# Performance work log

Measured on AMD Instinct MI355X. Metric: run time of the kernel, lower is better.

## Reference

```python
import jax, jax.numpy as jnp
import numpy as np
import math

B, L, D, P = 2, 2048, 256, 32
PI = math.pi


def _layernorm(x, g, b, eps=1e-5):
    m = x.mean(-1, keepdims=True)
    v = x.var(-1, keepdims=True)
    return (x - m) / jnp.sqrt(v + eps) * g + b


def setup_inputs() -> dict:
    key = jax.random.key(0)
    ks = jax.random.split(key, 16)
    sd = 1.0 / math.sqrt(D)
    f32 = jnp.float32
    inp = {
        "x": jax.random.normal(ks[0], (B, L, D), f32),
        # key_encoder: Linear(D, P)
        "key_W": jax.random.normal(ks[1], (D, P), f32) * sd,
        "key_b": jnp.zeros((P,), f32),
        # value_encoder: Linear(D, D)
        "val_W": jax.random.normal(ks[2], (D, D), f32) * sd,
        "val_b": jnp.zeros((D,), f32),
        # refiner: LayerNorm(D), Linear(D, 2D), GELU, Linear(2D, D)
        "ln1_g": jnp.ones((D,), f32),
        "ln1_b": jnp.zeros((D,), f32),
        "W1": jax.random.normal(ks[3], (D, 2 * D), f32) * sd,
        "b1": jnp.zeros((2 * D,), f32),
        "W2": jax.random.normal(ks[4], (2 * D, D), f32) * (1.0 / math.sqrt(2 * D)),
        "b2": jnp.zeros((D,), f32),
        # to_out: LayerNorm(D), Linear(D, D)
        "ln2_g": jnp.ones((D,), f32),
        "ln2_b": jnp.zeros((D,), f32),
        "Wo": jax.random.normal(ks[5], (D, D), f32) * sd,
        "bo": jnp.zeros((D,), f32),
    }
    return inp


def reference(x, key_W, key_b, val_W, val_b, ln1_g, ln1_b, W1, b1, W2, b2,
              ln2_g, ln2_b, Wo, bo):
    # key phases in (-pi, pi); phasor exp(i*theta) handled as (cos, sin)
    phases = jnp.tanh(x @ key_W + key_b) * PI          # (B, L, P)
    values = x @ val_W + val_b                          # (B, L, D)

    cos_p = jnp.cos(phases)
    sin_p = jnp.sin(phases)
    # torch.roll(shifts=1, dims=1) then zero the first position -> shift right, row 0 = 0
    zrow = jnp.zeros_like(cos_p[:, :1])
    cos_s = jnp.concatenate([zrow, cos_p[:, :-1]], axis=1)
    sin_s = jnp.concatenate([zrow, sin_p[:, :-1]], axis=1)

    # odd positions hold values
    vmask = (jnp.arange(L) % 2 == 1).astype(x.dtype)    # (L,)
    mv = values * vmask[None, :, None]                  # (B, L, D)

    # bind: outer product phasor (P) x value (D); real/imag parts
    bound_re = cos_s[..., None] * mv[:, :, None, :]     # (B, L, P, D)
    bound_im = sin_s[..., None] * mv[:, :, None, :]
    mem_re = jnp.cumsum(bound_re, axis=1)
    mem_im = jnp.cumsum(bound_im, axis=1)

    # retrieve: Re[ memory * exp(-i*theta) ] summed over phases
    retrieved = (jnp.einsum('blpd,blp->bld', mem_re, cos_p)
                 + jnp.einsum('blpd,blp->bld', mem_im, sin_p))

    valid = jnp.maximum(jnp.cumsum(vmask), 1.0)         # (L,)
    retrieved = retrieved / (jnp.sqrt(valid)[None, :, None] * math.sqrt(P))

    h = _layernorm(retrieved, ln1_g, ln1_b)
    h = jax.nn.gelu(h @ W1 + b1, approximate=False)
    refined = h @ W2 + b2
    out = x + (_layernorm(refined, ln2_g, ln2_b) @ Wo + bo)
    return out
```

## Files before the change

kernel.cpp:

```cpp
#include <hip/hip_runtime.h>
#include <math.h>

#define BB 2
#define LL 2048
#define DD 256
#define PP 32
#define NC 64
#define PI_F 3.14159265358979323846f

typedef __attribute__((ext_vector_type(8))) short bf16x8;
typedef __attribute__((ext_vector_type(4))) float f32x4;
typedef unsigned short ushort_t;
typedef unsigned int uint_t;

__device__ inline ushort_t f2bf(float x) {
    uint_t u = __float_as_uint(x);
    uint_t r = (u + 0x7fffu + ((u >> 16) & 1u)) >> 16;
    return (ushort_t)r;
}

__global__ __launch_bounds__(256) void prep_key_kernel(
    const float* __restrict__ W1, const float* __restrict__ W2,
    const float* __restrict__ Wo, const float* __restrict__ valW,
    const float* __restrict__ x, const float* __restrict__ key_W,
    const float* __restrict__ key_b,
    ushort_t* __restrict__ W1t, ushort_t* __restrict__ W2t,
    ushort_t* __restrict__ Wot, ushort_t* __restrict__ valWt,
    float2* __restrict__ ph)
{
    const int bid = blockIdx.x;
    const int t = threadIdx.x;
    if (bid < 96) {
        __shared__ float T[64][65];
        const float* W; ushort_t* Wt; int K, N, tile;
        if (bid < 32)      { W = W1;   Wt = W1t;   K = 256; N = 512; tile = bid; }
        else if (bid < 64) { W = W2;   Wt = W2t;   K = 512; N = 256; tile = bid - 32; }
        else if (bid < 80) { W = Wo;   Wt = Wot;   K = 256; N = 256; tile = bid - 64; }
        else               { W = valW; Wt = valWt; K = 256; N = 256; tile = bid - 80; }
        const int ntiles = N / 64;
        const int k0 = (tile / ntiles) * 64, n0 = (tile % ntiles) * 64;
        {
            const int rr = t >> 2, cb = (t & 3) * 16;
            #pragma unroll
            for (int i = 0; i < 16; i += 4) {
                const float4 v = *(const float4*)&W[(k0 + rr) * N + n0 + cb + i];
                T[rr][cb + i + 0] = v.x; T[rr][cb + i + 1] = v.y;
                T[rr][cb + i + 2] = v.z; T[rr][cb + i + 3] = v.w;
            }
        }
        __syncthreads();
        {
            const int n = t >> 2, kb = (t & 3) * 16;
            #pragma unroll
            for (int i = 0; i < 16; ++i)
                Wt[(n0 + n) * K + k0 + kb + i] = f2bf(T[kb + i][n]);
        }
    } else {
        __shared__ ushort_t xt[16][264];
        __shared__ ushort_t kwT[32][264];
        __shared__ float rbuf[4][2][16][17];
        const int row0 = (bid - 96) * 16;
        {
            const int l = t >> 4, cb = (t & 15) * 16;
            const float* src = &x[(long)(row0 + l) * DD + cb];
            ushort_t tmp[16];
            #pragma unroll
            for (int i = 0; i < 4; ++i) {
                const float4 v = *(const float4*)&src[i * 4];
                tmp[i*4+0] = f2bf(v.x); tmp[i*4+1] = f2bf(v.y);
                tmp[i*4+2] = f2bf(v.z); tmp[i*4+3] = f2bf(v.w);
            }
            *(uint4*)&xt[l][cb]     = *(uint4*)&tmp[0];
            *(uint4*)&xt[l][cb + 8] = *(uint4*)&tmp[8];
        }
        {
            #pragma unroll
            for (int i = 0; i < 8; ++i) {
                const int idx4 = i * 256 + t;
                const int k = idx4 >> 3, pc = (idx4 & 7) * 4;
                const float4 v = *(const float4*)&key_W[k * 32 + pc];
                kwT[pc + 0][k] = f2bf(v.x);
                kwT[pc + 1][k] = f2bf(v.y);
                kwT[pc + 2][k] = f2bf(v.z);
                kwT[pc + 3][k] = f2bf(v.w);
            }
        }
        __syncthreads();
        const int wv = t >> 6, lane = t & 63;
        const int qd = lane >> 4, mc = lane & 15;
        f32x4 acc0 = {0.f,0.f,0.f,0.f}, acc1 = {0.f,0.f,0.f,0.f};
        #pragma unroll
        for (int ks = 0; ks < 2; ++ks) {
            const int ko = wv * 64 + ks * 32 + qd * 8;
            const bf16x8 a  = *(const bf16x8*)&xt[mc][ko];
            const bf16x8 b0 = *(const bf16x8*)&kwT[mc][ko];
            const bf16x8 b1 = *(const bf16x8*)&kwT[16 + mc][ko];
            acc0 = __builtin_amdgcn_mfma_f32_16x16x32_bf16(a, b0, acc0, 0, 0, 0);
            acc1 = __builtin_amdgcn_mfma_f32_16x16x32_bf16(a, b1, acc1, 0, 0, 0);
        }
        #pragma unroll
        for (int r = 0; r < 4; ++r) {
            rbuf[wv][0][qd * 4 + r][mc] = acc0[r];
            rbuf[wv][1][qd * 4 + r][mc] = acc1[r];
        }
        __syncthreads();
        #pragma unroll
        for (int rep = 0; rep < 2; ++rep) {
            const int idx = rep * 256 + t;
            const int p = idx & 31, l = idx >> 5;
            const int nf = p >> 4, mcol = p & 15;
            float a = key_b[p] + rbuf[0][nf][l][mcol] + rbuf[1][nf][l][mcol]
                    + rbuf[2][nf][l][mcol] + rbuf[3][nf][l][mcol];
            a = tanhf(a) * PI_F;
            float sn, cs;
            sincosf(a, &sn, &cs);
            ph[(long)(row0 + l) * PP + p] = make_float2(cs, sn);
        }
    }
}

__global__ __launch_bounds__(256) void valbind_kernel(
    const float* __restrict__ x, const float2* __restrict__ ph,
    const ushort_t* __restrict__ valWt, const float* __restrict__ val_b,
    ushort_t* __restrict__ VoddT, float* __restrict__ Mt)
{
    __shared__ ushort_t xsb[16][264];
    __shared__ ushort_t VdT[64][40];
    __shared__ ushort_t phsT[64][40];
    __shared__ float    Ms[64][68];

    const int tid = threadIdx.x;
    const int bid = blockIdx.x;
    const int b  = bid >> 8;
    const int c  = (bid >> 2) & 63;
    const int dq = bid & 3;
    const int base = b * LL;
    const int r0 = 32 * c;

    {
        const int j = tid >> 4, cb = (tid & 15) * 16;
        const float* src = &x[(long)(base + r0 + 2 * j + 1) * DD + cb];
        ushort_t tmp[16];
        #pragma unroll
        for (int i = 0; i < 4; ++i) {
            const float4 v = *(const float4*)&src[i * 4];
            tmp[i*4+0] = f2bf(v.x); tmp[i*4+1] = f2bf(v.y);
            tmp[i*4+2] = f2bf(v.z); tmp[i*4+3] = f2bf(v.w);
        }
        *(uint4*)&xsb[j][cb]     = *(uint4*)&tmp[0];
        *(uint4*)&xsb[j][cb + 8] = *(uint4*)&tmp[8];
    }
    {
        const int j = tid >> 4, qb = (tid & 15) * 4;
        const float4 v = *(const float4*)((const float*)ph +
                              (long)(base + r0 + 2 * j) * 64 + qb);
        phsT[qb + 0][j] = f2bf(v.x);
        phsT[qb + 1][j] = f2bf(v.y);
        phsT[qb + 2][j] = f2bf(v.z);
        phsT[qb + 3][j] = f2bf(v.w);
    }
    for (int e = tid; e < 64 * 16; e += 256) {
        phsT[e >> 4][16 + (e & 15)] = 0;
        VdT[e >> 4][16 + (e & 15)] = 0;
    }
    __syncthreads();

    const int wv = tid >> 6, lane = tid & 63;
    const int qd = lane >> 4, mc = lane & 15;

    f32x4 va = {0.f,0.f,0.f,0.f};
    const int dloc = wv * 16 + mc;
    const int ng = dq * 64 + dloc;
    const ushort_t* B0 = &valWt[(long)ng * 256];
    #pragma unroll
    for (int ks = 0; ks < 8; ++ks) {
        const bf16x8 a  = *(const bf16x8*)&xsb[mc][ks * 32 + qd * 8];
        const bf16x8 b0 = *(const bf16x8*)&B0[ks * 32 + qd * 8];
        va = __builtin_amdgcn_mfma_f32_16x16x32_bf16(a, b0, va, 0, 0, 0);
    }
    {
        const float bb = val_b[ng];
        #pragma unroll
        for (int r = 0; r < 4; ++r)
            VdT[dloc][qd * 4 + r] = f2bf(va[r] + bb);
    }
    __syncthreads();

    const bf16x8 a2 = *(const bf16x8*)&phsT[wv * 16 + mc][qd * 8];
    f32x4 macc[4];
    #pragma unroll
    for (int nf = 0; nf < 4; ++nf) {
        f32x4 z = {0.f,0.f,0.f,0.f};
        const bf16x8 b2 = *(const bf16x8*)&VdT[nf * 16 + mc][qd * 8];
        macc[nf] = __builtin_amdgcn_mfma_f32_16x16x32_bf16(a2, b2, z, 0, 0, 0);
    }
    #pragma unroll
    for (int nf = 0; nf < 4; ++nf) {
        #pragma unroll
        for (int r = 0; r < 4; ++r)
            Ms[nf * 16 + mc][wv * 16 + qd * 4 + r] = macc[nf][r];
    }
    __syncthreads();

    {
        float* dst = &Mt[((long)(b * NC + c) * 256 + dq * 64) * 64];
        #pragma unroll
        for (int p = 0; p < 4; ++p) {
            const int idx4 = p * 256 + tid;
            const int dl = idx4 >> 4, q4 = (idx4 & 15) * 4;
            *(float4*)&dst[dl * 64 + q4] = *(const float4*)&Ms[dl][q4];
        }
    }
    if (tid < 64) {
        ushort_t* vd = &VoddT[((long)(b * NC + c) * 256 + dq * 64 + tid) * 16];
        *(uint4*)&vd[0] = *(const uint4*)&VdT[tid][0];
        *(uint4*)&vd[8] = *(const uint4*)&VdT[tid][8];
    }
}

__global__ __launch_bounds__(256) void prefix_kernel(float* __restrict__ M)
{
    __shared__ float segsum[4][64];
    const int tid = threadIdx.x;
    const int b  = blockIdx.x >> 8;
    const int cg = blockIdx.x & 255;
    const int col = cg * 64 + (tid & 63);
    const int seg = tid >> 6;
    const long base = (long)b * NC * 16384 + col;

    float v[16], s = 0.f;
    #pragma unroll
    for (int i = 0; i < 16; ++i) {
        v[i] = M[base + (long)(seg * 16 + i) * 16384];
        s += v[i];
    }
    segsum[seg][tid & 63] = s;
    __syncthreads();
    float run = 0.f;
    #pragma unroll
    for (int sg = 0; sg < 3; ++sg)
        if (sg < seg) run += segsum[sg][tid & 63];
    #pragma unroll
    for (int i = 0; i < 16; ++i) {
        const long a = base + (long)(seg * 16 + i) * 16384;
        M[a] = run;
        run += v[i];
    }
}

__global__ __launch_bounds__(256) void retrieve_kernel(
    const float* __restrict__ ph, const float* __restrict__ Mpre,
    const ushort_t* __restrict__ VoddT,
    const float* __restrict__ ln1_g, const float* __restrict__ ln1_b,
    ushort_t* __restrict__ rhat)
{
    __shared__ ushort_t Bs_m[256][72];
    __shared__ ushort_t Bs_v[256][32];
    __shared__ ushort_t As_ph[16][72];
    __shared__ ushort_t Bs_sh[16][72];
    __shared__ ushort_t As_p[16][32];
    __shared__ float    ref[16][264];

    const int tid = threadIdx.x;
    const int b = blockIdx.x >> 7;
    const int c = (blockIdx.x >> 1) & 63;
    const int h = blockIdx.x & 1;
    const int l0g = 32 * c + 16 * h;
    const long rowbase = (long)b * LL + l0g;

    {
        const float* src = &Mpre[(long)(b * NC + c) * 16384];
        #pragma unroll
        for (int p = 0; p < 16; ++p) {
            const int idx4 = p * 256 + tid;
            const int d = idx4 >> 4, q4 = (idx4 & 15) * 4;
            const float4 v = *(const float4*)&src[idx4 * 4];
            ushort_t tmp[4] = {f2bf(v.x), f2bf(v.y), f2bf(v.z), f2bf(v.w)};
            *(uint2*)&Bs_m[d][q4] = *(uint2*)tmp;
        }
    }
    {
        const int r = tid >> 4, q4 = (tid & 15) * 4;
        const float4 v = *(const float4*)&ph[(rowbase + r) * 64 + q4];
        ushort_t t0[4] = {f2bf(v.x), f2bf(v.y), f2bf(v.z), f2bf(v.w)};
        *(uint2*)&As_ph[r][q4] = *(uint2*)t0;
        const float4 w = *(const float4*)&ph[((long)b * LL + 32 * c + 2 * r) * 64 + q4];
        ushort_t t1[4] = {f2bf(w.x), f2bf(w.y), f2bf(w.z), f2bf(w.w)};
        *(uint2*)&Bs_sh[r][q4] = *(uint2*)t1;
    }
    {
        const ushort_t* src = &VoddT[(long)(b * NC + c) * 4096];
        const int j0 = (tid & 1) * 8;
        *(uint4*)&Bs_v[tid >> 1][j0] = *(const uint4*)&src[tid * 8];
        *(uint4*)&Bs_v[(tid + 256) >> 1][j0] = *(const uint4*)&src[(tid + 256) * 8];
        *(uint4*)&Bs_v[tid][16] = make_uint4(0, 0, 0, 0);
        *(uint4*)&Bs_v[tid][24] = make_uint4(0, 0, 0, 0);
        As_p[tid >> 4][16 + (tid & 15)] = 0;
    }
    __syncthreads();

    const int wv = tid >> 6, lane = tid & 63;
    const int qd = lane >> 4, mc = lane & 15;

    {
        f32x4 sacc = {0.f, 0.f, 0.f, 0.f};
        #pragma unroll
        for (int ks = 0; ks < 2; ++ks) {
            const bf16x8 a  = *(const bf16x8*)&As_ph[mc][ks * 32 + qd * 8];
            const bf16x8 bb = *(const bf16x8*)&Bs_sh[mc][ks * 32 + qd * 8];
            sacc = __builtin_amdgcn_mfma_f32_16x16x32_bf16(a, bb, sacc, 0, 0, 0);
        }
        if (wv == 0) {
            #pragma unroll
            for (int r = 0; r < 4; ++r) {
                const int l = qd * 4 + r;
                As_p[l][mc] = (2 * mc + 1 <= 16 * h + l) ? f2bf(sacc[r])
                                                         : (ushort_t)0;
            }
        }
    }

    f32x4 acc[4];
    #pragma unroll
    for (int i = 0; i < 4; ++i) acc[i] = (f32x4){0.f, 0.f, 0.f, 0.f};
    #pragma unroll
    for (int i = 0; i < 4; ++i) {
        const int d0 = wv * 64 + i * 16;
        #pragma unroll
        for (int ks = 0; ks < 2; ++ks) {
            const bf16x8 a  = *(const bf16x8*)&As_ph[mc][ks * 32 + qd * 8];
            const bf16x8 bb = *(const bf16x8*)&Bs_m[d0 + mc][ks * 32 + qd * 8];
            acc[i] = __builtin_amdgcn_mfma_f32_16x16x32_bf16(a, bb, acc[i], 0, 0, 0);
        }
    }
    __syncthreads();

    {
        const bf16x8 a2 = *(const bf16x8*)&As_p[mc][qd * 8];
        #pragma unroll
        for (int i = 0; i < 4; ++i) {
            const int d0 = wv * 64 + i * 16;
            const bf16x8 b2 = *(const bf16x8*)&Bs_v[d0 + mc][qd * 8];
            acc[i] = __builtin_amdgcn_mfma_f32_16x16x32_bf16(a2, b2, acc[i], 0, 0, 0);
        }
    }

    #pragma unroll
    for (int r = 0; r < 4; ++r) {
        const int l = qd * 4 + r;
        int va = (l0g + l + 1) >> 1; if (va < 1) va = 1;
        const float sc = 0.17677669529663687f * rsqrtf((float)va);
        #pragma unroll
        for (int i = 0; i < 4; ++i)
            ref[l][wv * 64 + i * 16 + mc] = acc[i][r] * sc;
    }
    __syncthreads();

    {
        const int row = tid >> 4, cg = (tid & 15) * 16;
        float s = 0.f, sq = 0.f;
        #pragma unroll
        for (int i = 0; i < 16; ++i) {
            const float v = ref[row][cg + i];
            s += v; sq += v * v;
        }
        s += __shfl_xor(s, 1, 16);  sq += __shfl_xor(sq, 1, 16);
        s += __shfl_xor(s, 2, 16);  sq += __shfl_xor(sq, 2, 16);
        s += __shfl_xor(s, 4, 16);  sq += __shfl_xor(sq, 4, 16);
        s += __shfl_xor(s, 8, 16);  sq += __shfl_xor(sq, 8, 16);
        const float m = s * (1.f / 256.f);
        const float inv = rsqrtf(sq * (1.f / 256.f) - m * m + 1e-5f);
        ushort_t o16[16];
        #pragma unroll
        for (int i = 0; i < 16; ++i) {
            const int cc = cg + i;
            o16[i] = f2bf((ref[row][cc] - m) * inv * ln1_g[cc] + ln1_b[cc]);
        }
        ushort_t* dst = &rhat[(rowbase + row) * DD + cg];
        *(uint4*)&dst[0] = *(uint4*)&o16[0];
        *(uint4*)&dst[8] = *(uint4*)&o16[8];
    }
}

template<int K, int N, int MODE>
__global__ __launch_bounds__(256) void mfma_gemm32(
    const ushort_t* __restrict__ A, const ushort_t* __restrict__ Bt,
    const float* __restrict__ bias, const float* __restrict__ resid,
    void* __restrict__ out)
{
    __shared__ ushort_t As[32][136];
    __shared__ ushort_t Bs[64][136];
    const int tid = threadIdx.x;
    const int mt = blockIdx.x & 127;
    const int nt = blockIdx.x >> 7;
    const int m0 = mt * 32, n0 = nt * 64;
    const int wv = tid >> 6, lane = tid & 63;
    const int qd = lane >> 4, mc = lane & 15;

    f32x4 acc0 = {0.f, 0.f, 0.f, 0.f};
    f32x4 acc1 = {0.f, 0.f, 0.f, 0.f};

    const int ar = tid >> 3, ak = (tid & 7) * 16;
    const int bn = tid >> 2, bk = (tid & 3) * 32;

    for (int k0 = 0; k0 < K; k0 += 128) {
        __syncthreads();
        {
            const ushort_t* sa = &A[(long)(m0 + ar) * K + k0 + ak];
            *(uint4*)&As[ar][ak]     = *(const uint4*)&sa[0];
            *(uint4*)&As[ar][ak + 8] = *(const uint4*)&sa[8];
        }
        {
            const ushort_t* src = &Bt[(long)(n0 + bn) * K + k0 + bk];
            *(uint4*)&Bs[bn][bk +  0] = *(const uint4*)&src[0];
            *(uint4*)&Bs[bn][bk +  8] = *(const uint4*)&src[8];
            *(uint4*)&Bs[bn][bk + 16] = *(const uint4*)&src[16];
            *(uint4*)&Bs[bn][bk + 24] = *(const uint4*)&src[24];
        }
        __syncthreads();
        #pragma unroll
        for (int ko = 0; ko < 128; ko += 32) {
            const bf16x8 a0 = *(const bf16x8*)&As[mc][ko + qd * 8];
            const bf16x8 a1 = *(const bf16x8*)&As[16 + mc][ko + qd * 8];
            const bf16x8 b  = *(const bf16x8*)&Bs[wv * 16 + mc][ko + qd * 8];
            acc0 = __builtin_amdgcn_mfma_f32_16x16x32_bf16(a0, b, acc0, 0, 0, 0);
            acc1 = __builtin_amdgcn_mfma_f32_16x16x32_bf16(a1, b, acc1, 0, 0, 0);
        }
    }

    const int nn = n0 + wv * 16 + mc;
    const float bb = bias[nn];
    #pragma unroll
    for (int r = 0; r < 4; ++r) {
        const long row0w = m0 + qd * 4 + r;
        const long row1w = row0w + 16;
        float v0 = acc0[r] + bb;
        float v1 = acc1[r] + bb;
        if (MODE == 0) {
            v0 = 0.5f * v0 * (1.f + erff(v0 * 0.70710678118654752f));
            v1 = 0.5f * v1 * (1.f + erff(v1 * 0.70710678118654752f));
            ((ushort_t*)out)[row0w * N + nn] = f2bf(v0);
            ((ushort_t*)out)[row1w * N + nn] = f2bf(v1);
        } else {
            ((float*)out)[row0w * N + nn] = v0 + resid[row0w * N + nn];
            ((float*)out)[row1w * N + nn] = v1 + resid[row1w * N + nn];
        }
    }
}

__global__ __launch_bounds__(256) void gemm2ln_kernel(
    const ushort_t* __restrict__ h, const ushort_t* __restrict__ W2t,
    const float* __restrict__ b2, const float* __restrict__ ln2_g,
    const float* __restrict__ ln2_b, ushort_t* __restrict__ shat)
{
    __shared__ ushort_t As[16][72];
    __shared__ ushort_t Bs[256][72];
    __shared__ float Ct[16][264];

    const int tid = threadIdx.x;
    const int m0 = blockIdx.x * 16;
    const int wv = tid >> 6, lane = tid & 63;
    const int qd = lane >> 4, mc = lane & 15;

    f32x4 acc[4];
    #pragma unroll
    for (int nf = 0; nf < 4; ++nf) acc[nf] = (f32x4){0.f,0.f,0.f,0.f};

    const int sr = tid >> 3, sk = (tid & 7) * 8;

    for (int k0 = 0; k0 < 512; k0 += 64) {
        __syncthreads();
        if (tid < 128)
            *(uint4*)&As[sr][sk] = *(const uint4*)&h[(long)(m0 + sr) * 512 + k0 + sk];
        #pragma unroll
        for (int rr = 0; rr < 8; ++rr) {
            const int n = rr * 32 + (tid >> 3);
            *(uint4*)&Bs[n][sk] = *(const uint4*)&W2t[(long)n * 512 + k0 + sk];
        }
        __syncthreads();
        #pragma unroll
        for (int ks = 0; ks < 2; ++ks) {
            const bf16x8 a = *(const bf16x8*)&As[mc][ks * 32 + qd * 8];
            #pragma unroll
            for (int nf = 0; nf < 4; ++nf) {
                const bf16x8 b = *(const bf16x8*)&Bs[wv * 64 + nf * 16 + mc][ks * 32 + qd * 8];
                acc[nf] = __builtin_amdgcn_mfma_f32_16x16x32_bf16(a, b, acc[nf], 0, 0, 0);
            }
        }
    }

    #pragma unroll
    for (int nf = 0; nf < 4; ++nf) {
        const int n = wv * 64 + nf * 16 + mc;
        const float bb = b2[n];
        #pragma unroll
        for (int r = 0; r < 4; ++r)
            Ct[qd * 4 + r][n] = acc[nf][r] + bb;
    }
    __syncthreads();

    {
        const int row = tid >> 4, cg = (tid & 15) * 16;
        float s = 0.f, sq = 0.f;
        #pragma unroll
        for (int i = 0; i < 16; ++i) {
            const float v = Ct[row][cg + i];
            s += v; sq += v * v;
        }
        s  += __shfl_xor(s, 1, 16);  sq += __shfl_xor(sq, 1, 16);
        s  += __shfl_xor(s, 2, 16);  sq += __shfl_xor(sq, 2, 16);
        s  += __shfl_xor(s, 4, 16);  sq += __shfl_xor(sq, 4, 16);
        s  += __shfl_xor(s, 8, 16);  sq += __shfl_xor(sq, 8, 16);
        const float m = s * (1.f / 256.f);
        const float inv = rsqrtf(sq * (1.f / 256.f) - m * m + 1e-5f);
        #pragma unroll
        for (int i = 0; i < 16; ++i) {
            const int cc = cg + i;
            shat[(long)(m0 + row) * DD + cc] =
                f2bf((Ct[row][cc] - m) * inv * ln2_g[cc] + ln2_b[cc]);
        }
    }
}

extern "C" void kernel_launch(void* const* d_in, const int* in_sizes, int n_in,
                              void* d_out, int out_size, void* d_ws, size_t ws_size,
                              hipStream_t stream)
{
    const float* x     = (const float*)d_in[0];
    const float* key_W = (const float*)d_in[1];
    const float* key_b = (const float*)d_in[2];
    const float* val_W = (const float*)d_in[3];
    const float* val_b = (const float*)d_in[4];
    const float* ln1_g = (const float*)d_in[5];
    const float* ln1_b = (const float*)d_in[6];
    const float* W1    = (const float*)d_in[7];
    const float* b1    = (const float*)d_in[8];
    const float* W2    = (const float*)d_in[9];
    const float* b2    = (const float*)d_in[10];
    const float* ln2_g = (const float*)d_in[11];
    const float* ln2_b = (const float*)d_in[12];
    const float* Wo    = (const float*)d_in[13];
    const float* bo    = (const float*)d_in[14];
    float* outp = (float*)d_out;

    float* ws = (float*)d_ws;
    float*  ph      = ws;
    float*  Mt      = ws + 262144;
    ushort_t* VoddT = (ushort_t*)(Mt + 2097152);
    ushort_t* rhat_b = VoddT + 524288;
    ushort_t* W1t   = rhat_b + 1048576;
    ushort_t* W2t   = W1t + 131072;
    ushort_t* Wot   = W2t + 131072;
    ushort_t* valWt = Wot + 65536;
    ushort_t* h_b    = (ushort_t*)Mt;
    ushort_t* shat_b = (ushort_t*)(Mt + 1048576);

    prep_key_kernel<<<352, 256, 0, stream>>>(W1, W2, Wo, val_W, x, key_W, key_b,
                                             W1t, W2t, Wot, valWt, (float2*)ph);
    valbind_kernel<<<512, 256, 0, stream>>>(x, (const float2*)ph, valWt, val_b,
                                            VoddT, Mt);
    prefix_kernel<<<512, 256, 0, stream>>>(Mt);
    retrieve_kernel<<<256, 256, 0, stream>>>(ph, Mt, VoddT, ln1_g, ln1_b, rhat_b);
    mfma_gemm32<256, 512, 0><<<1024, 256, 0, stream>>>(rhat_b, W1t, b1, nullptr, h_b);
    gemm2ln_kernel<<<256, 256, 0, stream>>>(h_b, W2t, b2, ln2_g, ln2_b, shat_b);
    mfma_gemm32<256, 256, 2><<<512, 256, 0, stream>>>(shat_b, Wot, bo, x, outp);
}
```

Measured before the change: 130.4 us.

## Fuse output projection into gemm2+LN kernel and store prefix memory as bf16

The prefix-scan kernel now writes the exclusive prefix sums directly as bf16 into a separate buffer, so the retrieve kernel loads half the bytes and skips its own conversion. The final Wo projection with bias and residual add is fused into the gemm2+LayerNorm kernel, which keeps the normalized row block in shared memory instead of writing and re-reading it from global memory. This removes one launch and one intermediate round trip. The cost is extra shared memory and lower parallelism for the Wo GEMM, which now runs on 256 blocks instead of 512.

```diff
diff --git a/kernel.cpp b/kernel.cpp
--- a/kernel.cpp
+++ b/kernel.cpp
@@ -218,7 +218,8 @@
     }
 }
 
-__global__ __launch_bounds__(256) void prefix_kernel(float* __restrict__ M)
+__global__ __launch_bounds__(256) void prefix_kernel(
+    const float* __restrict__ M, ushort_t* __restrict__ Mpre_b)
 {
     __shared__ float segsum[4][64];
     const int tid = threadIdx.x;
@@ -243,13 +244,13 @@
     #pragma unroll
     for (int i = 0; i < 16; ++i) {
         const long a = base + (long)(seg * 16 + i) * 16384;
-        M[a] = run;
+        Mpre_b[a] = f2bf(run);
         run += v[i];
     }
 }
 
 __global__ __launch_bounds__(256) void retrieve_kernel(
-    const float* __restrict__ ph, const float* __restrict__ Mpre,
+    const float* __restrict__ ph, const ushort_t* __restrict__ Mpre_b,
     const ushort_t* __restrict__ VoddT,
     const float* __restrict__ ln1_g, const float* __restrict__ ln1_b,
     ushort_t* __restrict__ rhat)
@@ -269,14 +270,12 @@
     const long rowbase = (long)b * LL + l0g;
 
     {
-        const float* src = &Mpre[(long)(b * NC + c) * 16384];
-        #pragma unroll
-        for (int p = 0; p < 16; ++p) {
-            const int idx4 = p * 256 + tid;
-            const int d = idx4 >> 4, q4 = (idx4 & 15) * 4;
-            const float4 v = *(const float4*)&src[idx4 * 4];
-            ushort_t tmp[4] = {f2bf(v.x), f2bf(v.y), f2bf(v.z), f2bf(v.w)};
-            *(uint2*)&Bs_m[d][q4] = *(uint2*)tmp;
+        const ushort_t* src = &Mpre_b[(long)(b * NC + c) * 16384];
+        #pragma unroll
+        for (int p = 0; p < 8; ++p) {
+            const int idx8 = p * 256 + tid;
+            const int d = idx8 >> 3, q8 = (idx8 & 7) * 8;
+            *(uint4*)&Bs_m[d][q8] = *(const uint4*)&src[idx8 * 8];
         }
     }
     {
@@ -382,11 +381,9 @@
     }
 }
 
-template<int K, int N, int MODE>
-__global__ __launch_bounds__(256) void mfma_gemm32(
+__global__ __launch_bounds__(256) void gemm1_kernel(
     const ushort_t* __restrict__ A, const ushort_t* __restrict__ Bt,
-    const float* __restrict__ bias, const float* __restrict__ resid,
-    void* __restrict__ out)
+    const float* __restrict__ bias, ushort_t* __restrict__ out)
 {
     __shared__ ushort_t As[32][136];
     __shared__ ushort_t Bs[64][136];
@@ -403,15 +400,15 @@
     const int ar = tid >> 3, ak = (tid & 7) * 16;
     const int bn = tid >> 2, bk = (tid & 3) * 32;
 
-    for (int k0 = 0; k0 < K; k0 += 128) {
+    for (int k0 = 0; k0 < 256; k0 += 128) {
         __syncthreads();
         {
-            const ushort_t* sa = &A[(long)(m0 + ar) * K + k0 + ak];
+            const ushort_t* sa = &A[(long)(m0 + ar) * 256 + k0 + ak];
             *(uint4*)&As[ar][ak]     = *(const uint4*)&sa[0];
             *(uint4*)&As[ar][ak + 8] = *(const uint4*)&sa[8];
         }
         {
-            const ushort_t* src = &Bt[(long)(n0 + bn) * K + k0 + bk];
+            const ushort_t* src = &Bt[(long)(n0 + bn) * 256 + k0 + bk];
             *(uint4*)&Bs[bn][bk +  0] = *(const uint4*)&src[0];
             *(uint4*)&Bs[bn][bk +  8] = *(const uint4*)&src[8];
             *(uint4*)&Bs[bn][bk + 16] = *(const uint4*)&src[16];
@@ -433,29 +430,26 @@
     #pragma unroll
     for (int r = 0; r < 4; ++r) {
         const long row0w = m0 + qd * 4 + r;
-        const long row1w = row0w + 16;
         float v0 = acc0[r] + bb;
         float v1 = acc1[r] + bb;
-        if (MODE == 0) {
-            v0 = 0.5f * v0 * (1.f + erff(v0 * 0.70710678118654752f));
-            v1 = 0.5f * v1 * (1.f + erff(v1 * 0.70710678118654752f));
-            ((ushort_t*)out)[row0w * N + nn] = f2bf(v0);
-            ((ushort_t*)out)[row1w * N + nn] = f2bf(v1);
-        } else {
-            ((float*)out)[row0w * N + nn] = v0 + resid[row0w * N + nn];
-            ((float*)out)[row1w * N + nn] = v1 + resid[row1w * N + nn];
-        }
-    }
-}
-
-__global__ __launch_bounds__(256) void gemm2ln_kernel(
+        v0 = 0.5f * v0 * (1.f + erff(v0 * 0.70710678118654752f));
+        v1 = 0.5f * v1 * (1.f + erff(v1 * 0.70710678118654752f));
+        out[row0w * 512 + nn] = f2bf(v0);
+        out[(row0w + 16) * 512 + nn] = f2bf(v1);
+    }
+}
+
+__global__ __launch_bounds__(256) void gemm23_kernel(
     const ushort_t* __restrict__ h, const ushort_t* __restrict__ W2t,
     const float* __restrict__ b2, const float* __restrict__ ln2_g,
-    const float* __restrict__ ln2_b, ushort_t* __restrict__ shat)
+    const float* __restrict__ ln2_b, const ushort_t* __restrict__ Wot,
+    const float* __restrict__ bo, const float* __restrict__ x,
+    float* __restrict__ out)
 {
     __shared__ ushort_t As[16][72];
     __shared__ ushort_t Bs[256][72];
     __shared__ float Ct[16][264];
+    __shared__ ushort_t shT[16][264];
 
     const int tid = threadIdx.x;
     const int m0 = blockIdx.x * 16;
@@ -516,8 +510,41 @@
         #pragma unroll
         for (int i = 0; i < 16; ++i) {
             const int cc = cg + i;
-            shat[(long)(m0 + row) * DD + cc] =
-                f2bf((Ct[row][cc] - m) * inv * ln2_g[cc] + ln2_b[cc]);
+            shT[row][cc] = f2bf((Ct[row][cc] - m) * inv * ln2_g[cc] + ln2_b[cc]);
+        }
+    }
+
+    f32x4 acc2[4];
+    #pragma unroll
+    for (int nf = 0; nf < 4; ++nf) acc2[nf] = (f32x4){0.f,0.f,0.f,0.f};
+
+    for (int k0 = 0; k0 < 256; k0 += 64) {
+        __syncthreads();
+        #pragma unroll
+        for (int rr = 0; rr < 8; ++rr) {
+            const int n = rr * 32 + (tid >> 3);
+            *(uint4*)&Bs[n][sk] = *(const uint4*)&Wot[(long)n * 256 + k0 + sk];
+        }
+        __syncthreads();
+        #pragma unroll
+        for (int ks = 0; ks < 2; ++ks) {
+            const bf16x8 a = *(const bf16x8*)&shT[mc][k0 + ks * 32 + qd * 8];
+            #pragma unroll
+            for (int nf = 0; nf < 4; ++nf) {
+                const bf16x8 b = *(const bf16x8*)&Bs[wv * 64 + nf * 16 + mc][ks * 32 + qd * 8];
+                acc2[nf] = __builtin_amdgcn_mfma_f32_16x16x32_bf16(a, b, acc2[nf], 0, 0, 0);
+            }
+        }
+    }
+
+    #pragma unroll
+    for (int nf = 0; nf < 4; ++nf) {
+        const int n = wv * 64 + nf * 16 + mc;
+        const float bb = bo[n];
+        #pragma unroll
+        for (int r = 0; r < 4; ++r) {
+            const long row = m0 + qd * 4 + r;
+            out[row * DD + n] = acc2[nf][r] + bb + x[row * DD + n];
         }
     }
 }
@@ -546,22 +573,22 @@
     float* ws = (float*)d_ws;
     float*  ph      = ws;
     float*  Mt      = ws + 262144;
-    ushort_t* VoddT = (ushort_t*)(Mt + 2097152);
+    ushort_t* Mpre_b = (ushort_t*)(Mt + 2097152);
+    ushort_t* VoddT  = Mpre_b + 2097152;
     ushort_t* rhat_b = VoddT + 524288;
     ushort_t* W1t   = rhat_b + 1048576;
     ushort_t* W2t   = W1t + 131072;
     ushort_t* Wot   = W2t + 131072;
     ushort_t* valWt = Wot + 65536;
     ushort_t* h_b    = (ushort_t*)Mt;
-    ushort_t* shat_b = (ushort_t*)(Mt + 1048576);
 
     prep_key_kernel<<<352, 256, 0, stream>>>(W1, W2, Wo, val_W, x, key_W, key_b,
                                              W1t, W2t, Wot, valWt, (float2*)ph);
     valbind_kernel<<<512, 256, 0, stream>>>(x, (const float2*)ph, valWt, val_b,
                                             VoddT, Mt);
-    prefix_kernel<<<512, 256, 0, stream>>>(Mt);
-    retrieve_kernel<<<256, 256, 0, stream>>>(ph, Mt, VoddT, ln1_g, ln1_b, rhat_b);
-    mfma_gemm32<256, 512, 0><<<1024, 256, 0, stream>>>(rhat_b, W1t, b1, nullptr, h_b);
-    gemm2ln_kernel<<<256, 256, 0, stream>>>(h_b, W2t, b2, ln2_g, ln2_b, shat_b);
-    mfma_gemm32<256, 256, 2><<<512, 256, 0, stream>>>(shat_b, Wot, bo, x, outp);
-}
+    prefix_kernel<<<512, 256, 0, stream>>>(Mt, Mpre_b);
+    retrieve_kernel<<<256, 256, 0, stream>>>(ph, Mpre_b, VoddT, ln1_g, ln1_b, rhat_b);
+    gemm1_kernel<<<1024, 256, 0, stream>>>(rhat_b, W1t, b1, h_b);
+    gemm23_kernel<<<256, 256, 0, stream>>>(h_b, W2t, b2, ln2_g, ln2_b,
+                                           Wot, bo, x, outp);
+}
```

After: 124.1 us. 1.05x faster.
